# Optimization experiments

Hardware: AMD Instinct MI355X
Metric: run time of the kernel (lower is better)

The kernel has to match this reference:

```python
import jax, jax.numpy as jnp
import numpy as np

HEAD = 8
D_Q = 64
NEG_INF = -1e9
EPS = 1e-9


def setup_inputs() -> dict:
    key = jax.random.key(0)
    ks = jax.random.split(key, 5)
    bs, seq_len, d_model = 4, 1024, 512
    context = jax.random.normal(ks[0], (bs, seq_len, d_model), dtype=jnp.float32)
    attention_mask = jnp.ones((bs, seq_len), dtype=jnp.int32)
    # nn.Linear default init: U(-1/sqrt(fan_in), 1/sqrt(fan_in))
    bound = 1.0 / np.sqrt(d_model)
    Wq = jax.random.uniform(ks[1], (HEAD * D_Q, d_model), jnp.float32, -bound, bound)
    bq = jax.random.uniform(ks[2], (HEAD * D_Q,), jnp.float32, -bound, bound)
    Wk = jax.random.uniform(ks[3], (HEAD * D_Q, d_model), jnp.float32, -bound, bound)
    bk = jax.random.uniform(ks[4], (HEAD * D_Q,), jnp.float32, -bound, bound)
    return {"context": context, "attention_mask": attention_mask,
            "Wq": Wq, "bq": bq, "Wk": Wk, "bk": bk}


def reference(context, attention_mask, Wq, bq, Wk, bk):
    bs, seq_len, d_model = context.shape
    # structural masks
    after_mask = jnp.eye(seq_len, k=1, dtype=jnp.int32)    # superdiagonal
    prev_mask = jnp.eye(seq_len, k=-1, dtype=jnp.int32)    # subdiagonal
    self_mask = jnp.eye(seq_len, dtype=jnp.int32)          # diagonal
    summing_op = jnp.triu(jnp.ones((seq_len, seq_len), jnp.float32))  # upper-tri ones

    # attention_mask & (after + prev): (bs,1,1,S) & (S,S) -> (bs,1,S,S)
    mask = attention_mask[:, None, None, :] & (after_mask + prev_mask)

    # projections -> (bs, head, seq, d_q)
    q = (context @ Wq.T + bq).reshape(bs, seq_len, HEAD, D_Q).transpose(0, 2, 1, 3)
    k = (context @ Wk.T + bk).reshape(bs, seq_len, HEAD, D_Q).transpose(0, 2, 1, 3)

    scores = jnp.einsum('bhqd,bhkd->bhqk', q, k) / d_model
    scores = jnp.where(mask == 0, NEG_INF, scores)
    scores = jax.nn.softmax(scores, axis=-1)

    # geometric-mean fusion of forward/backward neighbor scores
    phrasal_attn = jnp.sqrt(scores * jnp.swapaxes(scores, -2, -1) + EPS)
    # prior_attn = 0 (default): phrasal_attn = 0 + (1-0)*phrasal_attn

    # log-cumsum via triangular matmuls
    p = jnp.where(after_mask == 0, 0.0, jnp.log(phrasal_attn + EPS))  # (bs,h,S,S)
    p = jnp.einsum('bhij,jk->bhik', p, summing_op)
    attn = jnp.exp(jnp.einsum('ij,bhjk->bhik', summing_op, p))
    # zero out on-and-below diagonal (keep strict upper triangle)
    strict_upper = summing_op.astype(jnp.int32) - self_mask
    attn = jnp.where(strict_upper == 0, 0.0, attn)
    attn = attn + jnp.swapaxes(attn, -2, -1) + jnp.where(self_mask == 0, EPS, phrasal_attn)
    return (attn, phrasal_attn)
```

## Files before the change

kernel.cpp:

```cpp
#include <hip/hip_runtime.h>
#include <hip/hip_bf16.h>

#define BS 4
#define SEQ 1024
#define DM 512
#define EPS 1e-9f
#define SQRTEPS 3.16227766e-5f

typedef __attribute__((ext_vector_type(8))) short short8;
typedef __attribute__((ext_vector_type(4))) float floatx4;

__device__ __forceinline__ unsigned short f2bf(float x) {
    unsigned int u = __float_as_uint(x);
    return (unsigned short)((u + 0x7fffu + ((u >> 16) & 1u)) >> 16);
}

__device__ __forceinline__ void bgwrite(float* base, int n_iters, int tid, int nthr) {
    floatx4 v4 = {SQRTEPS, SQRTEPS, SQRTEPS, SQRTEPS};
    for (int j = 0; j < n_iters; ++j)
        *(floatx4*)(base + (size_t)(j * nthr + tid) * 4) = v4;
}

__global__ __launch_bounds__(256) void convert_kernel(
    const float* __restrict__ ctx, const float* __restrict__ Wq,
    const float* __restrict__ Wk, unsigned short* __restrict__ Xbf,
    unsigned short* __restrict__ Wbf, float* __restrict__ phrasal)
{
    const int blk = blockIdx.x, tid = threadIdx.x;
    if (blk >= 256) {
        bgwrite(phrasal + (size_t)(blk - 256) * 8192, 8, tid, 256);
        return;
    }
    int gthr = blk * 256 + tid;
    #pragma unroll
    for (int j = 0; j < 10; ++j) {
        int e4 = gthr + 65536 * j;
        int e  = e4 * 4;
        floatx4 s;
        if (e < 2097152) {
            s = *(const floatx4*)(ctx + e);
        } else {
            int e2 = e - 2097152;
            s = (e2 < 262144) ? *(const floatx4*)(Wq + e2)
                              : *(const floatx4*)(Wk + e2 - 262144);
        }
        ushort2 lo = {f2bf(s.x), f2bf(s.y)}, hi = {f2bf(s.z), f2bf(s.w)};
        unsigned short* dst = (e < 2097152) ? (Xbf + e) : (Wbf + e - 2097152);
        *(ushort2*)dst = lo;
        *(ushort2*)(dst + 2) = hi;
    }
}

#define NGEMM 512
#define LDW 72
#define LDQ 65

__global__ __launch_bounds__(256) void gemmdot_kernel(
    const unsigned short* __restrict__ Xbf, const unsigned short* __restrict__ Wbf,
    const float* __restrict__ bq, const float* __restrict__ bk,
    float* __restrict__ uA, float* __restrict__ vA,
    float* __restrict__ qF, float* __restrict__ kF,
    float* __restrict__ qL, float* __restrict__ kL,
    float* __restrict__ phrasal)
{
    __shared__ char smem[2 * 64 * LDQ * 4];
    unsigned short* Xs  = (unsigned short*)smem;
    unsigned short* Wqs = Xs + 64 * LDW;
    unsigned short* Wks = Wqs + 64 * LDW;
    float* qS = (float*)smem;
    float* kS = qS + 64 * LDQ;

    const int blk = blockIdx.x, tid = threadIdx.x;
    if (blk >= NGEMM) {
        bgwrite(phrasal + (size_t)(768 + blk - NGEMM) * 8192, 8, tid, 256);
        return;
    }

    const int rt = blk >> 3, h = blk & 7;
    const int wv = tid >> 6, lane = tid & 63;
    const int lr = lane & 15, kg = lane >> 4;

    const int r0 = tid >> 3, kc0 = (tid & 7) << 3;
    const unsigned short* Xb  = Xbf + (size_t)(rt * 64) * DM;
    const unsigned short* Wqb = Wbf + (size_t)(h * 64) * DM;
    const unsigned short* Wkb = Wbf + 262144 + (size_t)(h * 64) * DM;

    floatx4 acc_q[4] = {}, acc_k[4] = {};

    for (int k0 = 0; k0 < DM; k0 += 64) {
        uint4 x0  = *(const uint4*)(Xb  + (size_t)r0 * DM + k0 + kc0);
        uint4 x1  = *(const uint4*)(Xb  + (size_t)(r0 + 32) * DM + k0 + kc0);
        uint4 wq0 = *(const uint4*)(Wqb + (size_t)r0 * DM + k0 + kc0);
        uint4 wq1 = *(const uint4*)(Wqb + (size_t)(r0 + 32) * DM + k0 + kc0);
        uint4 wk0 = *(const uint4*)(Wkb + (size_t)r0 * DM + k0 + kc0);
        uint4 wk1 = *(const uint4*)(Wkb + (size_t)(r0 + 32) * DM + k0 + kc0);
        __syncthreads();
        *(uint4*)(Xs  + r0 * LDW + kc0)        = x0;
        *(uint4*)(Xs  + (r0 + 32) * LDW + kc0) = x1;
        *(uint4*)(Wqs + r0 * LDW + kc0)        = wq0;
        *(uint4*)(Wqs + (r0 + 32) * LDW + kc0) = wq1;
        *(uint4*)(Wks + r0 * LDW + kc0)        = wk0;
        *(uint4*)(Wks + (r0 + 32) * LDW + kc0) = wk1;
        __syncthreads();
        #pragma unroll
        for (int ks = 0; ks < 2; ++ks) {
            short8 a = *(const short8*)(Xs + (wv * 16 + lr) * LDW + ks * 32 + kg * 8);
            #pragma unroll
            for (int ni = 0; ni < 4; ++ni) {
                short8 bqf = *(const short8*)(Wqs + (ni * 16 + lr) * LDW + ks * 32 + kg * 8);
                acc_q[ni] = __builtin_amdgcn_mfma_f32_16x16x32_bf16(a, bqf, acc_q[ni], 0, 0, 0);
                short8 bkf = *(const short8*)(Wks + (ni * 16 + lr) * LDW + ks * 32 + kg * 8);
                acc_k[ni] = __builtin_amdgcn_mfma_f32_16x16x32_bf16(a, bkf, acc_k[ni], 0, 0, 0);
            }
        }
    }

    __syncthreads();
    #pragma unroll
    for (int ni = 0; ni < 4; ++ni) {
        float bqv = bq[h * 64 + ni * 16 + lr];
        float bkv = bk[h * 64 + ni * 16 + lr];
        #pragma unroll
        for (int r = 0; r < 4; ++r) {
            int row = wv * 16 + kg * 4 + r;
            qS[row * LDQ + ni * 16 + lr] = acc_q[ni][r] + bqv;
            kS[row * LDQ + ni * 16 + lr] = acc_k[ni][r] + bkv;
        }
    }
    __syncthreads();

    const int eb = (rt * 8 + h) * 64;
    if (tid < 64) {
        qF[eb + tid] = qS[tid];
        kF[eb + tid] = kS[tid];
    } else if (tid >= 192) {
        int l = tid - 192;
        qL[eb + l] = qS[63 * LDQ + l];
        kL[eb + l] = kS[63 * LDQ + l];
    }

    for (int p = wv; p < 63; p += 4) {
        float pu = qS[p * LDQ + lane] * kS[(p + 1) * LDQ + lane];
        float pv = qS[(p + 1) * LDQ + lane] * kS[p * LDQ + lane];
        #pragma unroll
        for (int m = 1; m < 64; m <<= 1) {
            pu += __shfl_xor(pu, m);
            pv += __shfl_xor(pv, m);
        }
        if (lane == 0) {
            int r = rt * 64 + p;
            int idx = (((r >> 10) * 8 + h) << 10) | (r & 1023);
            uA[idx] = pu * (1.0f / DM);
            vA[idx] = pv * (1.0f / DM);
        }
    }
}

__global__ __launch_bounds__(1024) void gscan_kernel(
    const float* __restrict__ uA, const float* __restrict__ vA,
    const float* __restrict__ qF, const float* __restrict__ kF,
    const float* __restrict__ qL, const float* __restrict__ kL,
    const int* __restrict__ am, float* __restrict__ gA, float* __restrict__ CA,
    float* __restrict__ phrasal)
{
    __shared__ float uS[SEQ], vS[SEQ];
    __shared__ float uFix[16], vFix[16];
    __shared__ double wsum[16];

    const int blk = blockIdx.x, i = threadIdx.x;
    if (blk >= 32) {
        bgwrite(phrasal + (size_t)(2816 + blk - 32) * 8192, 2, i, 1024);
        return;
    }

    const int bh = blk, b = bh >> 3, h = bh & 7;
    const int base = bh * SEQ;
    const int wv = i >> 6, lane = i & 63;

    uS[i] = uA[base + i];
    vS[i] = vA[base + i];

    if (wv < 15) {
        int e0 = ((b * 16 + wv) * 8 + h) * 64;
        int e1 = e0 + 8 * 64;
        float pu = qL[e0 + lane] * kF[e1 + lane];
        float pv = qF[e1 + lane] * kL[e0 + lane];
        #pragma unroll
        for (int m = 1; m < 64; m <<= 1) {
            pu += __shfl_xor(pu, m);
            pv += __shfl_xor(pv, m);
        }
        if (lane == 0) { uFix[wv] = pu * (1.0f / DM); vFix[wv] = pv * (1.0f / DM); }
    }
    __syncthreads();
    if ((i & 63) == 63) {
        int j = i >> 6;
        uS[i] = (j < 15) ? uFix[j] : 0.f;
        vS[i] = (j < 15) ? vFix[j] : 0.f;
    }
    __syncthreads();

    float g = 0.f;
    if (i < SEQ - 1) {
        float u = uS[i], vv = vS[i];
        float vm1 = (i > 0) ? vS[i - 1] : 0.f;
        float up1 = uS[i + 1];
        const int* amb = am + b * SEQ;
        int mL = (i > 0) ? amb[i - 1] : 0;
        int mR = amb[i + 1];
        float s_up = mR ? (mL ? 1.f / (1.f + expf(vm1 - u)) : 1.f) : 0.f;
        int mL2 = amb[i];
        int mR2 = (i + 2 < SEQ) ? amb[i + 2] : 0;
        float s_dn = mL2 ? (mR2 ? 1.f / (1.f + expf(up1 - vv)) : 1.f) : 0.f;
        g = sqrtf(s_up * s_dn + EPS);
        gA[base + i] = g;
    }

    double L = (i < SEQ - 1) ? (double)logf(g + EPS) : 0.0;
    double x = L;
    #pragma unroll
    for (int off = 1; off < 64; off <<= 1) {
        double t = __shfl_up(x, off);
        if (lane >= off) x += t;
    }
    if (lane == 63) wsum[wv] = x;
    __syncthreads();
    double pref = 0.0;
    for (int w = 0; w < wv; ++w) pref += wsum[w];
    CA[base + i] = (float)(pref + x - L);
}

__global__ __launch_bounds__(256) void fill_attn(
    const float* __restrict__ gA, const float* __restrict__ CA,
    float* __restrict__ attn, float* __restrict__ phrasal)
{
    const int row = blockIdx.x;
    const int bh  = row >> 10;
    const int i   = row & 1023;
    const int t   = threadIdx.x;

    const float Ci = CA[row];
    floatx4 c4 = *(const floatx4*)(CA + bh * SEQ + t * 4);
    floatx4 av;
    #pragma unroll
    for (int j = 0; j < 4; ++j) {
        int k = t * 4 + j;
        float d = (k > i) ? (c4[j] - Ci) : (Ci - c4[j]);
        av[j] = (k == i) ? SQRTEPS : (__expf(d) + EPS);
    }
    *(floatx4*)(attn + (size_t)row * SEQ + t * 4) = av;

    if (t == 0 && i > 0)
        phrasal[(size_t)row * SEQ + i - 1] = gA[bh * SEQ + i - 1];
    if (t == 1 && i < SEQ - 1)
        phrasal[(size_t)row * SEQ + i + 1] = gA[bh * SEQ + i];
}

extern "C" void kernel_launch(void* const* d_in, const int* in_sizes, int n_in,
                              void* d_out, int out_size, void* d_ws, size_t ws_size,
                              hipStream_t stream) {
    const float* ctx = (const float*)d_in[0];
    const int*   am  = (const int*)d_in[1];
    const float* Wq  = (const float*)d_in[2];
    const float* bq  = (const float*)d_in[3];
    const float* Wk  = (const float*)d_in[4];
    const float* bk  = (const float*)d_in[5];
    float* out = (float*)d_out;

    char* ws = (char*)d_ws;
    unsigned short* Xbf = (unsigned short*)(ws);
    unsigned short* Wbf = (unsigned short*)(ws + 4194304);
    float*          uA  = (float*)(ws + 5242880);
    float*          vA  = (float*)(ws + 5373952);
    float*          gA  = (float*)(ws + 5505024);
    float*          CA  = (float*)(ws + 5636096);
    float*          qF  = (float*)(ws + 5767168);
    float*          kF  = (float*)(ws + 5898240);
    float*          qL  = (float*)(ws + 6029312);
    float*          kL  = (float*)(ws + 6160384);

    float* attn_out    = out;
    float* phrasal_out = out + (size_t)BS * 8 * SEQ * SEQ;

    convert_kernel<<<dim3(256 + 768), 256, 0, stream>>>(ctx, Wq, Wk, Xbf, Wbf, phrasal_out);
    gemmdot_kernel<<<dim3(NGEMM + 2048), 256, 0, stream>>>(
        Xbf, Wbf, bq, bk, uA, vA, qF, kF, qL, kL, phrasal_out);
    gscan_kernel<<<dim3(32 + 1280), 1024, 0, stream>>>(
        uA, vA, qF, kF, qL, kL, am, gA, CA, phrasal_out);
    fill_attn<<<dim3(BS * 8 * SEQ), 256, 0, stream>>>(gA, CA, attn_out, phrasal_out);
}
```

Baseline: 290.7 us.

## Fuse bf16 conversion and scan into GEMM kernel via last-block atomic counter

Drops the separate fp32-to-bf16 conversion kernel: the GEMM now loads fp32 context and weights directly and converts them while staging into shared memory. The scan kernel is also folded into the GEMM kernel. An atomic per-(batch,head) counter picks the last of the 16 row-tile blocks, and that block does the neighbour fixups, the sigmoid/log computation and the prefix sum, with 256 threads handling 4 elements each. This removes two kernel launches and the bf16 workspace round trip. In exchange it adds a memset, re-converts the weights in every block, and serializes the scan tail onto a few blocks.

```diff
diff --git a/kernel.cpp b/kernel.cpp
--- a/kernel.cpp
+++ b/kernel.cpp
@@ -6,101 +6,90 @@
 #define DM 512
 #define EPS 1e-9f
 #define SQRTEPS 3.16227766e-5f
+#define NGEMM 512
+#define NBG 4096
+#define LDW 72
+#define LDQ 65
 
 typedef __attribute__((ext_vector_type(8))) short short8;
 typedef __attribute__((ext_vector_type(4))) float floatx4;
 
-__device__ __forceinline__ unsigned short f2bf(float x) {
-    unsigned int u = __float_as_uint(x);
-    return (unsigned short)((u + 0x7fffu + ((u >> 16) & 1u)) >> 16);
-}
-
-__device__ __forceinline__ void bgwrite(float* base, int n_iters, int tid, int nthr) {
+__device__ __forceinline__ void bgwrite(float* base, int n_iters, int tid) {
     floatx4 v4 = {SQRTEPS, SQRTEPS, SQRTEPS, SQRTEPS};
     for (int j = 0; j < n_iters; ++j)
-        *(floatx4*)(base + (size_t)(j * nthr + tid) * 4) = v4;
-}
-
-__global__ __launch_bounds__(256) void convert_kernel(
-    const float* __restrict__ ctx, const float* __restrict__ Wq,
-    const float* __restrict__ Wk, unsigned short* __restrict__ Xbf,
-    unsigned short* __restrict__ Wbf, float* __restrict__ phrasal)
-{
-    const int blk = blockIdx.x, tid = threadIdx.x;
-    if (blk >= 256) {
-        bgwrite(phrasal + (size_t)(blk - 256) * 8192, 8, tid, 256);
-        return;
-    }
-    int gthr = blk * 256 + tid;
-    #pragma unroll
-    for (int j = 0; j < 10; ++j) {
-        int e4 = gthr + 65536 * j;
-        int e  = e4 * 4;
-        floatx4 s;
-        if (e < 2097152) {
-            s = *(const floatx4*)(ctx + e);
-        } else {
-            int e2 = e - 2097152;
-            s = (e2 < 262144) ? *(const floatx4*)(Wq + e2)
-                              : *(const floatx4*)(Wk + e2 - 262144);
-        }
-        ushort2 lo = {f2bf(s.x), f2bf(s.y)}, hi = {f2bf(s.z), f2bf(s.w)};
-        unsigned short* dst = (e < 2097152) ? (Xbf + e) : (Wbf + e - 2097152);
-        *(ushort2*)dst = lo;
-        *(ushort2*)(dst + 2) = hi;
-    }
-}
-
-#define NGEMM 512
-#define LDW 72
-#define LDQ 65
+        *(floatx4*)(base + (size_t)(j * 256 + tid) * 4) = v4;
+}
+
+__device__ __forceinline__ void cvst16(unsigned short* dst, floatx4 a, floatx4 b) {
+    union { __hip_bfloat162 h2[4]; uint4 u; } r;
+    r.h2[0] = __float22bfloat162_rn(make_float2(a.x, a.y));
+    r.h2[1] = __float22bfloat162_rn(make_float2(a.z, a.w));
+    r.h2[2] = __float22bfloat162_rn(make_float2(b.x, b.y));
+    r.h2[3] = __float22bfloat162_rn(make_float2(b.z, b.w));
+    *(uint4*)dst = r.u;
+}
 
 __global__ __launch_bounds__(256) void gemmdot_kernel(
-    const unsigned short* __restrict__ Xbf, const unsigned short* __restrict__ Wbf,
+    const float* __restrict__ ctx,
+    const float* __restrict__ Wq, const float* __restrict__ Wk,
     const float* __restrict__ bq, const float* __restrict__ bk,
+    const int* __restrict__ am,
     float* __restrict__ uA, float* __restrict__ vA,
     float* __restrict__ qF, float* __restrict__ kF,
     float* __restrict__ qL, float* __restrict__ kL,
-    float* __restrict__ phrasal)
+    float* __restrict__ gA, float* __restrict__ CA,
+    unsigned* __restrict__ cnt, float* __restrict__ phrasal)
 {
     __shared__ char smem[2 * 64 * LDQ * 4];
+    __shared__ float uFix[16], vFix[16];
+    __shared__ double wsum[4];
+    __shared__ int lastS;
+
     unsigned short* Xs  = (unsigned short*)smem;
     unsigned short* Wqs = Xs + 64 * LDW;
     unsigned short* Wks = Wqs + 64 * LDW;
     float* qS = (float*)smem;
     float* kS = qS + 64 * LDQ;
+    float* uS = (float*)smem;
+    float* vS = uS + SEQ;
 
     const int blk = blockIdx.x, tid = threadIdx.x;
     if (blk >= NGEMM) {
-        bgwrite(phrasal + (size_t)(768 + blk - NGEMM) * 8192, 8, tid, 256);
+        bgwrite(phrasal + (size_t)(blk - NGEMM) * 8192, 8, tid);
         return;
     }
 
     const int rt = blk >> 3, h = blk & 7;
     const int wv = tid >> 6, lane = tid & 63;
     const int lr = lane & 15, kg = lane >> 4;
-
     const int r0 = tid >> 3, kc0 = (tid & 7) << 3;
-    const unsigned short* Xb  = Xbf + (size_t)(rt * 64) * DM;
-    const unsigned short* Wqb = Wbf + (size_t)(h * 64) * DM;
-    const unsigned short* Wkb = Wbf + 262144 + (size_t)(h * 64) * DM;
+
+    const float* Xb  = ctx + (size_t)(rt * 64) * DM;
+    const float* Wqb = Wq + (size_t)(h * 64) * DM;
+    const float* Wkb = Wk + (size_t)(h * 64) * DM;
 
     floatx4 acc_q[4] = {}, acc_k[4] = {};
 
     for (int k0 = 0; k0 < DM; k0 += 64) {
-        uint4 x0  = *(const uint4*)(Xb  + (size_t)r0 * DM + k0 + kc0);
-        uint4 x1  = *(const uint4*)(Xb  + (size_t)(r0 + 32) * DM + k0 + kc0);
-        uint4 wq0 = *(const uint4*)(Wqb + (size_t)r0 * DM + k0 + kc0);
-        uint4 wq1 = *(const uint4*)(Wqb + (size_t)(r0 + 32) * DM + k0 + kc0);
-        uint4 wk0 = *(const uint4*)(Wkb + (size_t)r0 * DM + k0 + kc0);
-        uint4 wk1 = *(const uint4*)(Wkb + (size_t)(r0 + 32) * DM + k0 + kc0);
+        const float* xp0 = Xb  + (size_t)r0 * DM + k0 + kc0;
+        const float* xp1 = Xb  + (size_t)(r0 + 32) * DM + k0 + kc0;
+        const float* qp0 = Wqb + (size_t)r0 * DM + k0 + kc0;
+        const float* qp1 = Wqb + (size_t)(r0 + 32) * DM + k0 + kc0;
+        const float* kp0 = Wkb + (size_t)r0 * DM + k0 + kc0;
+        const float* kp1 = Wkb + (size_t)(r0 + 32) * DM + k0 + kc0;
+        floatx4 xa = *(const floatx4*)xp0, xb = *(const floatx4*)(xp0 + 4);
+        floatx4 xc = *(const floatx4*)xp1, xd = *(const floatx4*)(xp1 + 4);
+        floatx4 qa = *(const floatx4*)qp0, qb = *(const floatx4*)(qp0 + 4);
+        floatx4 qc = *(const floatx4*)qp1, qd = *(const floatx4*)(qp1 + 4);
+        floatx4 ka = *(const floatx4*)kp0, kb = *(const floatx4*)(kp0 + 4);
+        floatx4 kc = *(const floatx4*)kp1, kd = *(const floatx4*)(kp1 + 4);
         __syncthreads();
-        *(uint4*)(Xs  + r0 * LDW + kc0)        = x0;
-        *(uint4*)(Xs  + (r0 + 32) * LDW + kc0) = x1;
-        *(uint4*)(Wqs + r0 * LDW + kc0)        = wq0;
-        *(uint4*)(Wqs + (r0 + 32) * LDW + kc0) = wq1;
-        *(uint4*)(Wks + r0 * LDW + kc0)        = wk0;
-        *(uint4*)(Wks + (r0 + 32) * LDW + kc0) = wk1;
+        cvst16(Xs  + r0 * LDW + kc0, xa, xb);
+        cvst16(Xs  + (r0 + 32) * LDW + kc0, xc, xd);
+        cvst16(Wqs + r0 * LDW + kc0, qa, qb);
+        cvst16(Wqs + (r0 + 32) * LDW + kc0, qc, qd);
+        cvst16(Wks + r0 * LDW + kc0, ka, kb);
+        cvst16(Wks + (r0 + 32) * LDW + kc0, kc, kd);
         __syncthreads();
         #pragma unroll
         for (int ks = 0; ks < 2; ++ks) {
@@ -154,35 +143,28 @@
             vA[idx] = pv * (1.0f / DM);
         }
     }
-}
-
-__global__ __launch_bounds__(1024) void gscan_kernel(
-    const float* __restrict__ uA, const float* __restrict__ vA,
-    const float* __restrict__ qF, const float* __restrict__ kF,
-    const float* __restrict__ qL, const float* __restrict__ kL,
-    const int* __restrict__ am, float* __restrict__ gA, float* __restrict__ CA,
-    float* __restrict__ phrasal)
-{
-    __shared__ float uS[SEQ], vS[SEQ];
-    __shared__ float uFix[16], vFix[16];
-    __shared__ double wsum[16];
-
-    const int blk = blockIdx.x, i = threadIdx.x;
-    if (blk >= 32) {
-        bgwrite(phrasal + (size_t)(2816 + blk - 32) * 8192, 2, i, 1024);
-        return;
-    }
-
-    const int bh = blk, b = bh >> 3, h = bh & 7;
+
+    const int bh = (rt >> 4) * 8 + h;
+    __syncthreads();
+    if (tid == 0) {
+        unsigned old = __hip_atomic_fetch_add(cnt + bh, 1u,
+                           __ATOMIC_ACQ_REL, __HIP_MEMORY_SCOPE_AGENT);
+        lastS = (old == 15);
+    }
+    __syncthreads();
+    if (!lastS) return;
+    __threadfence();
+
     const int base = bh * SEQ;
-    const int wv = i >> 6, lane = i & 63;
-
-    uS[i] = uA[base + i];
-    vS[i] = vA[base + i];
-
-    if (wv < 15) {
-        int e0 = ((b * 16 + wv) * 8 + h) * 64;
-        int e1 = e0 + 8 * 64;
+    #pragma unroll
+    for (int j = 0; j < 4; ++j) {
+        int i = tid + 256 * j;
+        uS[i] = uA[base + i];
+        vS[i] = vA[base + i];
+    }
+    for (int p = wv; p < 15; p += 4) {
+        int rt0 = (rt >> 4) * 16 + p;
+        int e0 = (rt0 * 8 + h) * 64, e1 = e0 + 512;
         float pu = qL[e0 + lane] * kF[e1 + lane];
         float pv = qF[e1 + lane] * kL[e0 + lane];
         #pragma unroll
@@ -190,34 +172,42 @@
             pu += __shfl_xor(pu, m);
             pv += __shfl_xor(pv, m);
         }
-        if (lane == 0) { uFix[wv] = pu * (1.0f / DM); vFix[wv] = pv * (1.0f / DM); }
-    }
-    __syncthreads();
-    if ((i & 63) == 63) {
-        int j = i >> 6;
-        uS[i] = (j < 15) ? uFix[j] : 0.f;
-        vS[i] = (j < 15) ? vFix[j] : 0.f;
-    }
-    __syncthreads();
-
-    float g = 0.f;
-    if (i < SEQ - 1) {
-        float u = uS[i], vv = vS[i];
-        float vm1 = (i > 0) ? vS[i - 1] : 0.f;
-        float up1 = uS[i + 1];
-        const int* amb = am + b * SEQ;
-        int mL = (i > 0) ? amb[i - 1] : 0;
-        int mR = amb[i + 1];
-        float s_up = mR ? (mL ? 1.f / (1.f + expf(vm1 - u)) : 1.f) : 0.f;
-        int mL2 = amb[i];
-        int mR2 = (i + 2 < SEQ) ? amb[i + 2] : 0;
-        float s_dn = mL2 ? (mR2 ? 1.f / (1.f + expf(up1 - vv)) : 1.f) : 0.f;
-        g = sqrtf(s_up * s_dn + EPS);
-        gA[base + i] = g;
-    }
-
-    double L = (i < SEQ - 1) ? (double)logf(g + EPS) : 0.0;
-    double x = L;
+        if (lane == 0) { uFix[p] = pu * (1.0f / DM); vFix[p] = pv * (1.0f / DM); }
+    }
+    __syncthreads();
+    if (tid < 16) {
+        int i = tid * 64 + 63;
+        uS[i] = (tid < 15) ? uFix[tid] : 0.f;
+        vS[i] = (tid < 15) ? vFix[tid] : 0.f;
+    }
+    __syncthreads();
+
+    const int* amb = am + (rt >> 4) * SEQ;
+    const int i0 = tid * 4;
+    floatx4 g4;
+    double pref[4], tsum = 0.0;
+    #pragma unroll
+    for (int j = 0; j < 4; ++j) {
+        int i = i0 + j;
+        float g = 0.f;
+        if (i < SEQ - 1) {
+            float u = uS[i], vv = vS[i];
+            float vm1 = (i > 0) ? vS[i - 1] : 0.f;
+            float up1 = uS[i + 1];
+            int mL = (i > 0) ? amb[i - 1] : 0;
+            int mR = amb[i + 1];
+            float s_up = mR ? (mL ? 1.f / (1.f + expf(vm1 - u)) : 1.f) : 0.f;
+            int mL2 = amb[i];
+            int mR2 = (i + 2 < SEQ) ? amb[i + 2] : 0;
+            float s_dn = mL2 ? (mR2 ? 1.f / (1.f + expf(up1 - vv)) : 1.f) : 0.f;
+            g = sqrtf(s_up * s_dn + EPS);
+        }
+        g4[j] = g;
+        float L = (i < SEQ - 1) ? logf(g + EPS) : 0.f;
+        pref[j] = tsum;
+        tsum += (double)L;
+    }
+    double x = tsum;
     #pragma unroll
     for (int off = 1; off < 64; off <<= 1) {
         double t = __shfl_up(x, off);
@@ -225,9 +215,14 @@
     }
     if (lane == 63) wsum[wv] = x;
     __syncthreads();
-    double pref = 0.0;
-    for (int w = 0; w < wv; ++w) pref += wsum[w];
-    CA[base + i] = (float)(pref + x - L);
+    double woff = 0.0;
+    for (int w = 0; w < wv; ++w) woff += wsum[w];
+    double ex = woff + x - tsum;
+    floatx4 C4;
+    #pragma unroll
+    for (int j = 0; j < 4; ++j) C4[j] = (float)(ex + pref[j]);
+    *(floatx4*)(CA + base + i0) = C4;
+    *(floatx4*)(gA + base + i0) = g4;
 }
 
 __global__ __launch_bounds__(256) void fill_attn(
@@ -268,24 +263,21 @@
     float* out = (float*)d_out;
 
     char* ws = (char*)d_ws;
-    unsigned short* Xbf = (unsigned short*)(ws);
-    unsigned short* Wbf = (unsigned short*)(ws + 4194304);
-    float*          uA  = (float*)(ws + 5242880);
-    float*          vA  = (float*)(ws + 5373952);
-    float*          gA  = (float*)(ws + 5505024);
-    float*          CA  = (float*)(ws + 5636096);
-    float*          qF  = (float*)(ws + 5767168);
-    float*          kF  = (float*)(ws + 5898240);
-    float*          qL  = (float*)(ws + 6029312);
-    float*          kL  = (float*)(ws + 6160384);
+    float*    uA  = (float*)(ws);
+    float*    vA  = (float*)(ws + 131072);
+    float*    gA  = (float*)(ws + 262144);
+    float*    CA  = (float*)(ws + 393216);
+    float*    qF  = (float*)(ws + 524288);
+    float*    kF  = (float*)(ws + 655360);
+    float*    qL  = (float*)(ws + 786432);
+    float*    kL  = (float*)(ws + 917504);
+    unsigned* cnt = (unsigned*)(ws + 1048576);
 
     float* attn_out    = out;
     float* phrasal_out = out + (size_t)BS * 8 * SEQ * SEQ;
 
-    convert_kernel<<<dim3(256 + 768), 256, 0, stream>>>(ctx, Wq, Wk, Xbf, Wbf, phrasal_out);
-    gemmdot_kernel<<<dim3(NGEMM + 2048), 256, 0, stream>>>(
-        Xbf, Wbf, bq, bk, uA, vA, qF, kF, qL, kL, phrasal_out);
-    gscan_kernel<<<dim3(32 + 1280), 1024, 0, stream>>>(
-        uA, vA, qF, kF, qL, kL, am, gA, CA, phrasal_out);
+    hipMemsetAsync(cnt, 0, 128, stream);
+    gemmdot_kernel<<<dim3(NGEMM + NBG), 256, 0, stream>>>(
+        ctx, Wq, Wk, bq, bk, am, uA, vA, qF, kF, qL, kL, gA, CA, cnt, phrasal_out);
     fill_attn<<<dim3(BS * 8 * SEQ), 256, 0, stream>>>(gA, CA, attn_out, phrasal_out);
 }
```

Result: slower. 319.2 us (+9.8%).
